# Optimization experiments

Hardware: AMD Instinct MI355X
Metric: run time of the kernel (lower is better)

Reference implementation:

```python
import jax, jax.numpy as jnp
import numpy as np

T, B, D = 4096, 64, 64
SCALE = D ** (-0.5)


def setup_inputs() -> dict:
    key = jax.random.key(0)
    ks = jax.random.split(key, 8)
    init = 1.0 / np.sqrt(D)  # mimic nn.Linear default scale roughly
    return {
        "eeg": jax.random.normal(ks[0], (T, B, D), dtype=jnp.float32),
        "fnirs": jax.random.normal(ks[1], (T, B, D), dtype=jnp.float32),
        "Wq": jax.random.normal(ks[2], (D, D), dtype=jnp.float32) * init,
        "bq": jax.random.normal(ks[3], (D,), dtype=jnp.float32) * init,
        "Wk": jax.random.normal(ks[4], (D, D), dtype=jnp.float32) * init,
        "bk": jax.random.normal(ks[5], (D,), dtype=jnp.float32) * init,
        "Wv": jax.random.normal(ks[6], (D, D), dtype=jnp.float32) * init,
        "bv": jax.random.normal(ks[7], (D,), dtype=jnp.float32) * init,
    }


def reference(eeg, fnirs, Wq, bq, Wk, bk, Wv, bv):
    # Linear layers: x @ W.T + b (torch nn.Linear convention, W is [out, in])
    q = jnp.einsum("tbd,od->tbo", eeg, Wq) + bq      # [T, B, D]
    k = jnp.einsum("tbd,od->tbo", fnirs, Wk) + bk    # [T, B, D]
    v = jnp.einsum("tbd,od->tbo", fnirs, Wv) + bv    # [T, B, D]
    # Elementwise QK gating score, summed over feature dim -> [T, B, 1]
    score = jnp.sum(q * k, axis=-1, keepdims=True) * SCALE
    # Softmax over the sequence axis (dim=0)
    attn = jax.nn.softmax(score, axis=0)
    # Residual combine
    return eeg + attn * v
```

## Files before the change

kernel.cpp:

```cpp
#include <hip/hip_runtime.h>
#include <hip/hip_bf16.h>
#include <math.h>

#define T_DIM 4096
#define B_DIM 64
#define D_DIM 64
#define NROWS (T_DIM * B_DIM)
#define NTILES (NROWS / 16)

#define WS_M     0
#define WS_W     4096
#define WS_U     4160
#define WS_C     4224
#define WS_SCORE 8192

typedef __attribute__((ext_vector_type(4))) float f32x4;
typedef __attribute__((ext_vector_type(8))) short bf16x8;

static __device__ inline short f2bf(float x) {
  union { float f; unsigned u; } v; v.f = x;
  return (short)((v.u + 0x7FFFu + ((v.u >> 16) & 1u)) >> 16);
}

static __device__ inline bf16x8 load_cvt8(const float* __restrict__ p) {
  const float4 a = *reinterpret_cast<const float4*>(p);
  const float4 b = *reinterpret_cast<const float4*>(p + 4);
  bf16x8 r;
  r[0] = f2bf(a.x); r[1] = f2bf(a.y); r[2] = f2bf(a.z); r[3] = f2bf(a.w);
  r[4] = f2bf(b.x); r[5] = f2bf(b.y); r[6] = f2bf(b.z); r[7] = f2bf(b.w);
  return r;
}

__global__ __launch_bounds__(64) void k1_precompute(
    const float* __restrict__ Wq, const float* __restrict__ bq,
    const float* __restrict__ Wk, const float* __restrict__ bk,
    float* __restrict__ ws) {
  const int tid = threadIdx.x;
  const int blk = blockIdx.x;
  if (blk < 64) {
    const int d = blk;
    float acc = 0.f;
    for (int o = 0; o < 64; ++o)
      acc = fmaf(Wq[o * 64 + d], Wk[o * 64 + tid], acc);
    ws[WS_M + d * 64 + tid] = acc;
  } else {
    float uacc = 0.f, wacc = 0.f, cacc = 0.f;
    for (int o = 0; o < 64; ++o) {
      uacc = fmaf(bq[o], Wk[o * 64 + tid], uacc);
      wacc = fmaf(Wq[o * 64 + tid], bk[o], wacc);
      cacc = fmaf(bq[o], bk[o], cacc);
    }
    ws[WS_U + tid] = uacc;
    ws[WS_W + tid] = wacc;
    if (tid == 0) ws[WS_C] = cacc;
  }
}

__global__ __launch_bounds__(256, 4) void k2_score_mfma(
    const float* __restrict__ eeg, const float* __restrict__ fnirs,
    const float* __restrict__ Mm, const float* __restrict__ wvec,
    const float* __restrict__ uvec, const float* __restrict__ cvec,
    float* __restrict__ score) {
  const int lane = threadIdx.x & 63;
  const int wv   = threadIdx.x >> 6;
  const int wid  = blockIdx.x * 4 + wv;
  const int nwav = gridDim.x * 4;
  const int col  = lane & 15;
  const int grp  = lane >> 4;
  const int kb   = grp * 8;

  bf16x8 bf[5][2];
#pragma unroll
  for (int ct = 0; ct < 4; ++ct) {
    const int c = ct * 16 + col;
#pragma unroll
    for (int kf = 0; kf < 2; ++kf)
      bf[ct][kf] = load_cvt8(Mm + c * 64 + kf * 32 + kb);
  }
#pragma unroll
  for (int kf = 0; kf < 2; ++kf) {
    bf16x8 z = (bf16x8)(short)0;
    if (col == 0) z = load_cvt8(uvec + kf * 32 + kb);
    bf[4][kf] = z;
  }
  const float wreg[4] = { wvec[col], wvec[16 + col], wvec[32 + col], wvec[48 + col] };
  const float cb = cvec[0];
  const f32x4 zero = {0.f, 0.f, 0.f, 0.f};

  for (int tile = wid; tile < NTILES; tile += nwav) {
    const int rbase = tile * 16;
    const float* fa = fnirs + (size_t)(rbase + col) * 64 + kb;
    const bf16x8 a0 = load_cvt8(fa);
    const bf16x8 a1 = load_cvt8(fa + 32);
    f32x4 acc[5];
#pragma unroll
    for (int ct = 0; ct < 5; ++ct) {
      acc[ct] = __builtin_amdgcn_mfma_f32_16x16x32_bf16(a0, bf[ct][0], zero, 0, 0, 0);
      acc[ct] = __builtin_amdgcn_mfma_f32_16x16x32_bf16(a1, bf[ct][1], acc[ct], 0, 0, 0);
    }
    float partial[4];
#pragma unroll
    for (int i = 0; i < 4; ++i) {
      const int row = rbase + grp * 4 + i;
      float s = 0.f;
#pragma unroll
      for (int ct = 0; ct < 4; ++ct) {
        const float e = eeg[(size_t)row * 64 + ct * 16 + col];
        s = fmaf(e, acc[ct][i] + wreg[ct], s);
      }
      if (col == 0) s += acc[4][i] + cb;
      partial[i] = s;
    }
#pragma unroll
    for (int m = 8; m >= 1; m >>= 1) {
#pragma unroll
      for (int i = 0; i < 4; ++i)
        partial[i] += __shfl_xor(partial[i], m, 64);
    }
    if (col == 0) {
      float4 o = { partial[0] * 0.125f, partial[1] * 0.125f,
                   partial[2] * 0.125f, partial[3] * 0.125f };
      *reinterpret_cast<float4*>(score + rbase + grp * 4) = o;
    }
  }
}

__global__ __launch_bounds__(256) void k3_softmax(float* __restrict__ sc) {
  __shared__ float red[8];
  __shared__ float sinv;
  const int b = blockIdx.x;
  const int tid = threadIdx.x;

  float vals[16];
  float m = -1e30f;
#pragma unroll
  for (int k = 0; k < 16; ++k) {
    vals[k] = sc[(size_t)(k * 256 + tid) * 64 + b];
    m = fmaxf(m, vals[k]);
  }
#pragma unroll
  for (int off = 32; off > 0; off >>= 1)
    m = fmaxf(m, __shfl_xor(m, off, 64));
  if ((tid & 63) == 0) red[tid >> 6] = m;
  __syncthreads();
  m = fmaxf(fmaxf(red[0], red[1]), fmaxf(red[2], red[3]));

  float s = 0.f;
#pragma unroll
  for (int k = 0; k < 16; ++k) s += __expf(vals[k] - m);
#pragma unroll
  for (int off = 32; off > 0; off >>= 1)
    s += __shfl_xor(s, off, 64);
  if ((tid & 63) == 0) red[4 + (tid >> 6)] = s;
  __syncthreads();
  if (tid == 0) sinv = 1.0f / (red[4] + red[5] + red[6] + red[7]);
  __syncthreads();
  const float inv = sinv;
#pragma unroll
  for (int k = 0; k < 16; ++k)
    sc[(size_t)(k * 256 + tid) * 64 + b] = __expf(vals[k] - m) * inv;
}

__global__ __launch_bounds__(256, 4) void k4_output_mfma(
    const float* __restrict__ eeg, const float* __restrict__ fnirs,
    const float* __restrict__ Wv, const float* __restrict__ bv,
    const float* __restrict__ attn, float* __restrict__ out) {
  const int lane = threadIdx.x & 63;
  const int wv   = threadIdx.x >> 6;
  const int wid  = blockIdx.x * 4 + wv;
  const int nwav = gridDim.x * 4;
  const int col  = lane & 15;
  const int grp  = lane >> 4;
  const int kb   = grp * 8;

  bf16x8 bf[4][2];
#pragma unroll
  for (int ct = 0; ct < 4; ++ct) {
    const int c = ct * 16 + col;
#pragma unroll
    for (int kf = 0; kf < 2; ++kf)
      bf[ct][kf] = load_cvt8(Wv + c * 64 + kf * 32 + kb);
  }
  const float bvreg[4] = { bv[col], bv[16 + col], bv[32 + col], bv[48 + col] };
  const f32x4 zero = {0.f, 0.f, 0.f, 0.f};

  for (int tile = wid; tile < NTILES; tile += nwav) {
    const int rbase = tile * 16;
    const float* fa = fnirs + (size_t)(rbase + col) * 64 + kb;
    const bf16x8 a0 = load_cvt8(fa);
    const bf16x8 a1 = load_cvt8(fa + 32);
    f32x4 acc[4];
#pragma unroll
    for (int ct = 0; ct < 4; ++ct) {
      acc[ct] = __builtin_amdgcn_mfma_f32_16x16x32_bf16(a0, bf[ct][0], zero, 0, 0, 0);
      acc[ct] = __builtin_amdgcn_mfma_f32_16x16x32_bf16(a1, bf[ct][1], acc[ct], 0, 0, 0);
    }
    const float4 a4 = *reinterpret_cast<const float4*>(attn + rbase + grp * 4);
    const float av[4] = { a4.x, a4.y, a4.z, a4.w };
#pragma unroll
    for (int i = 0; i < 4; ++i) {
      const size_t row = rbase + grp * 4 + i;
#pragma unroll
      for (int ct = 0; ct < 4; ++ct) {
        const float e = eeg[row * 64 + ct * 16 + col];
        out[row * 64 + ct * 16 + col] = fmaf(av[i], acc[ct][i] + bvreg[ct], e);
      }
    }
  }
}

extern "C" void kernel_launch(void* const* d_in, const int* in_sizes, int n_in,
                              void* d_out, int out_size, void* d_ws, size_t ws_size,
                              hipStream_t stream) {
  const float* eeg   = (const float*)d_in[0];
  const float* fnirs = (const float*)d_in[1];
  const float* Wq    = (const float*)d_in[2];
  const float* bq    = (const float*)d_in[3];
  const float* Wk    = (const float*)d_in[4];
  const float* bk    = (const float*)d_in[5];
  const float* Wv    = (const float*)d_in[6];
  const float* bv    = (const float*)d_in[7];
  float* out = (float*)d_out;
  float* ws  = (float*)d_ws;

  k1_precompute<<<65, 64, 0, stream>>>(Wq, bq, Wk, bk, ws);
  k2_score_mfma<<<1024, 256, 0, stream>>>(eeg, fnirs,
                                          ws + WS_M, ws + WS_W, ws + WS_U,
                                          ws + WS_C, ws + WS_SCORE);
  k3_softmax<<<64, 256, 0, stream>>>(ws + WS_SCORE);
  k4_output_mfma<<<1024, 256, 0, stream>>>(eeg, fnirs, Wv, bv,
                                           ws + WS_SCORE, out);
}
```

Measured before the change: 81.72 us.

## Precompute bf16 weights and use one-tile-per-wave grids with front-loaded loads

The precompute kernel now writes the folded QK matrix, the u vector and Wv as bf16 into the workspace. The score and output kernels load these bf16 fragments directly instead of converting fp32 weights in every wave. Both MFMA kernels drop the persistent grid-stride loop and launch one 16-row tile per wave (4096 blocks), issuing all fnirs, eeg and attn loads up front so more memory requests are in flight. The cost is more blocks and a repeated weight load per wave, plus eeg values held in registers.

Result: faster. 79.63 us (-2.6%).

```diff
diff --git a/kernel.cpp b/kernel.cpp
--- a/kernel.cpp
+++ b/kernel.cpp
@@ -8,9 +8,10 @@
 #define NROWS (T_DIM * B_DIM)
 #define NTILES (NROWS / 16)
 
-#define WS_M     0
-#define WS_W     4096
-#define WS_U     4160
+#define WS_MBF   0
+#define WS_VBF   2048
+#define WS_UBF   4096
+#define WS_W     4160
 #define WS_C     4224
 #define WS_SCORE 8192
 
@@ -18,13 +19,11 @@
 typedef __attribute__((ext_vector_type(8))) short bf16x8;
 
 static __device__ inline short f2bf(float x) {
-  union { float f; unsigned u; } v; v.f = x;
-  return (short)((v.u + 0x7FFFu + ((v.u >> 16) & 1u)) >> 16);
-}
-
-static __device__ inline bf16x8 load_cvt8(const float* __restrict__ p) {
-  const float4 a = *reinterpret_cast<const float4*>(p);
-  const float4 b = *reinterpret_cast<const float4*>(p + 4);
+  __hip_bfloat16 h = __float2bfloat16(x);
+  return *reinterpret_cast<short*>(&h);
+}
+
+static __device__ inline bf16x8 cvt8(const float4 a, const float4 b) {
   bf16x8 r;
   r[0] = f2bf(a.x); r[1] = f2bf(a.y); r[2] = f2bf(a.z); r[3] = f2bf(a.w);
   r[4] = f2bf(b.x); r[5] = f2bf(b.y); r[6] = f2bf(b.z); r[7] = f2bf(b.w);
@@ -34,15 +33,19 @@
 __global__ __launch_bounds__(64) void k1_precompute(
     const float* __restrict__ Wq, const float* __restrict__ bq,
     const float* __restrict__ Wk, const float* __restrict__ bk,
-    float* __restrict__ ws) {
+    const float* __restrict__ Wv, float* __restrict__ ws) {
   const int tid = threadIdx.x;
   const int blk = blockIdx.x;
+  unsigned short* __restrict__ mbf = (unsigned short*)(ws + WS_MBF);
+  unsigned short* __restrict__ vbf = (unsigned short*)(ws + WS_VBF);
+  unsigned short* __restrict__ ubf = (unsigned short*)(ws + WS_UBF);
   if (blk < 64) {
     const int d = blk;
     float acc = 0.f;
     for (int o = 0; o < 64; ++o)
       acc = fmaf(Wq[o * 64 + d], Wk[o * 64 + tid], acc);
-    ws[WS_M + d * 64 + tid] = acc;
+    mbf[d * 64 + tid] = (unsigned short)f2bf(acc);
+    vbf[d * 64 + tid] = (unsigned short)f2bf(Wv[d * 64 + tid]);
   } else {
     float uacc = 0.f, wacc = 0.f, cacc = 0.f;
     for (int o = 0; o < 64; ++o) {
@@ -50,7 +53,7 @@
       wacc = fmaf(Wq[o * 64 + tid], bk[o], wacc);
       cacc = fmaf(bq[o], bk[o], cacc);
     }
-    ws[WS_U + tid] = uacc;
+    ubf[tid] = (unsigned short)f2bf(uacc);
     ws[WS_W + tid] = wacc;
     if (tid == 0) ws[WS_C] = cacc;
   }
@@ -58,70 +61,75 @@
 
 __global__ __launch_bounds__(256, 4) void k2_score_mfma(
     const float* __restrict__ eeg, const float* __restrict__ fnirs,
-    const float* __restrict__ Mm, const float* __restrict__ wvec,
-    const float* __restrict__ uvec, const float* __restrict__ cvec,
+    const unsigned short* __restrict__ mbf, const float* __restrict__ wvec,
+    const unsigned short* __restrict__ ubf, const float* __restrict__ cvec,
     float* __restrict__ score) {
   const int lane = threadIdx.x & 63;
   const int wv   = threadIdx.x >> 6;
-  const int wid  = blockIdx.x * 4 + wv;
-  const int nwav = gridDim.x * 4;
+  const int tile = blockIdx.x * 4 + wv;
   const int col  = lane & 15;
   const int grp  = lane >> 4;
   const int kb   = grp * 8;
-
-  bf16x8 bf[5][2];
-#pragma unroll
-  for (int ct = 0; ct < 4; ++ct) {
-    const int c = ct * 16 + col;
+  const int rbase = tile * 16;
+
+  const float* fa = fnirs + (size_t)(rbase + col) * 64 + kb;
+  const float4 f0a = *reinterpret_cast<const float4*>(fa);
+  const float4 f0b = *reinterpret_cast<const float4*>(fa + 4);
+  const float4 f1a = *reinterpret_cast<const float4*>(fa + 32);
+  const float4 f1b = *reinterpret_cast<const float4*>(fa + 36);
+  float ee[4][4];
+#pragma unroll
+  for (int i = 0; i < 4; ++i)
+#pragma unroll
+    for (int ct = 0; ct < 4; ++ct)
+      ee[i][ct] = eeg[(size_t)(rbase + grp * 4 + i) * 64 + ct * 16 + col];
+
+  bf16x8 bm[5][2];
+#pragma unroll
+  for (int ct = 0; ct < 4; ++ct)
 #pragma unroll
     for (int kf = 0; kf < 2; ++kf)
-      bf[ct][kf] = load_cvt8(Mm + c * 64 + kf * 32 + kb);
-  }
+      bm[ct][kf] = *reinterpret_cast<const bf16x8*>(
+          mbf + (ct * 16 + col) * 64 + kf * 32 + kb);
 #pragma unroll
   for (int kf = 0; kf < 2; ++kf) {
     bf16x8 z = (bf16x8)(short)0;
-    if (col == 0) z = load_cvt8(uvec + kf * 32 + kb);
-    bf[4][kf] = z;
+    if (col == 0)
+      z = *reinterpret_cast<const bf16x8*>(ubf + kf * 32 + kb);
+    bm[4][kf] = z;
   }
   const float wreg[4] = { wvec[col], wvec[16 + col], wvec[32 + col], wvec[48 + col] };
   const float cb = cvec[0];
+
+  const bf16x8 a0 = cvt8(f0a, f0b);
+  const bf16x8 a1 = cvt8(f1a, f1b);
   const f32x4 zero = {0.f, 0.f, 0.f, 0.f};
-
-  for (int tile = wid; tile < NTILES; tile += nwav) {
-    const int rbase = tile * 16;
-    const float* fa = fnirs + (size_t)(rbase + col) * 64 + kb;
-    const bf16x8 a0 = load_cvt8(fa);
-    const bf16x8 a1 = load_cvt8(fa + 32);
-    f32x4 acc[5];
-#pragma unroll
-    for (int ct = 0; ct < 5; ++ct) {
-      acc[ct] = __builtin_amdgcn_mfma_f32_16x16x32_bf16(a0, bf[ct][0], zero, 0, 0, 0);
-      acc[ct] = __builtin_amdgcn_mfma_f32_16x16x32_bf16(a1, bf[ct][1], acc[ct], 0, 0, 0);
-    }
-    float partial[4];
-#pragma unroll
-    for (int i = 0; i < 4; ++i) {
-      const int row = rbase + grp * 4 + i;
-      float s = 0.f;
-#pragma unroll
-      for (int ct = 0; ct < 4; ++ct) {
-        const float e = eeg[(size_t)row * 64 + ct * 16 + col];
-        s = fmaf(e, acc[ct][i] + wreg[ct], s);
-      }
-      if (col == 0) s += acc[4][i] + cb;
-      partial[i] = s;
-    }
-#pragma unroll
-    for (int m = 8; m >= 1; m >>= 1) {
-#pragma unroll
-      for (int i = 0; i < 4; ++i)
-        partial[i] += __shfl_xor(partial[i], m, 64);
-    }
-    if (col == 0) {
-      float4 o = { partial[0] * 0.125f, partial[1] * 0.125f,
-                   partial[2] * 0.125f, partial[3] * 0.125f };
-      *reinterpret_cast<float4*>(score + rbase + grp * 4) = o;
-    }
+  f32x4 acc[5];
+#pragma unroll
+  for (int ct = 0; ct < 5; ++ct) {
+    acc[ct] = __builtin_amdgcn_mfma_f32_16x16x32_bf16(a0, bm[ct][0], zero, 0, 0, 0);
+    acc[ct] = __builtin_amdgcn_mfma_f32_16x16x32_bf16(a1, bm[ct][1], acc[ct], 0, 0, 0);
+  }
+
+  float partial[4];
+#pragma unroll
+  for (int i = 0; i < 4; ++i) {
+    float s = 0.f;
+#pragma unroll
+    for (int ct = 0; ct < 4; ++ct)
+      s = fmaf(ee[i][ct], acc[ct][i] + wreg[ct], s);
+    if (col == 0) s += acc[4][i] + cb;
+    partial[i] = s;
+  }
+#pragma unroll
+  for (int m = 8; m >= 1; m >>= 1)
+#pragma unroll
+    for (int i = 0; i < 4; ++i)
+      partial[i] += __shfl_xor(partial[i], m, 64);
+  if (col == 0) {
+    float4 o = { partial[0] * 0.125f, partial[1] * 0.125f,
+                 partial[2] * 0.125f, partial[3] * 0.125f };
+    *reinterpret_cast<float4*>(score + rbase + grp * 4) = o;
   }
 }
 
@@ -163,49 +171,55 @@
 
 __global__ __launch_bounds__(256, 4) void k4_output_mfma(
     const float* __restrict__ eeg, const float* __restrict__ fnirs,
-    const float* __restrict__ Wv, const float* __restrict__ bv,
+    const unsigned short* __restrict__ vbf, const float* __restrict__ bv,
     const float* __restrict__ attn, float* __restrict__ out) {
   const int lane = threadIdx.x & 63;
   const int wv   = threadIdx.x >> 6;
-  const int wid  = blockIdx.x * 4 + wv;
-  const int nwav = gridDim.x * 4;
+  const int tile = blockIdx.x * 4 + wv;
   const int col  = lane & 15;
   const int grp  = lane >> 4;
   const int kb   = grp * 8;
-
-  bf16x8 bf[4][2];
+  const int rbase = tile * 16;
+
+  const float* fa = fnirs + (size_t)(rbase + col) * 64 + kb;
+  const float4 f0a = *reinterpret_cast<const float4*>(fa);
+  const float4 f0b = *reinterpret_cast<const float4*>(fa + 4);
+  const float4 f1a = *reinterpret_cast<const float4*>(fa + 32);
+  const float4 f1b = *reinterpret_cast<const float4*>(fa + 36);
+  float ee[4][4];
+#pragma unroll
+  for (int i = 0; i < 4; ++i)
+#pragma unroll
+    for (int ct = 0; ct < 4; ++ct)
+      ee[i][ct] = eeg[(size_t)(rbase + grp * 4 + i) * 64 + ct * 16 + col];
+  const float4 a4 = *reinterpret_cast<const float4*>(attn + rbase + grp * 4);
+
+  bf16x8 bm[4][2];
+#pragma unroll
+  for (int ct = 0; ct < 4; ++ct)
+#pragma unroll
+    for (int kf = 0; kf < 2; ++kf)
+      bm[ct][kf] = *reinterpret_cast<const bf16x8*>(
+          vbf + (ct * 16 + col) * 64 + kf * 32 + kb);
+  const float bvreg[4] = { bv[col], bv[16 + col], bv[32 + col], bv[48 + col] };
+
+  const bf16x8 a0 = cvt8(f0a, f0b);
+  const bf16x8 a1 = cvt8(f1a, f1b);
+  const f32x4 zero = {0.f, 0.f, 0.f, 0.f};
+  f32x4 acc[4];
 #pragma unroll
   for (int ct = 0; ct < 4; ++ct) {
-    const int c = ct * 16 + col;
-#pragma unroll
-    for (int kf = 0; kf < 2; ++kf)
-      bf[ct][kf] = load_cvt8(Wv + c * 64 + kf * 32 + kb);
-  }
-  const float bvreg[4] = { bv[col], bv[16 + col], bv[32 + col], bv[48 + col] };
-  const f32x4 zero = {0.f, 0.f, 0.f, 0.f};
-
-  for (int tile = wid; tile < NTILES; tile += nwav) {
-    const int rbase = tile * 16;
-    const float* fa = fnirs + (size_t)(rbase + col) * 64 + kb;
-    const bf16x8 a0 = load_cvt8(fa);
-    const bf16x8 a1 = load_cvt8(fa + 32);
-    f32x4 acc[4];
-#pragma unroll
-    for (int ct = 0; ct < 4; ++ct) {
-      acc[ct] = __builtin_amdgcn_mfma_f32_16x16x32_bf16(a0, bf[ct][0], zero, 0, 0, 0);
-      acc[ct] = __builtin_amdgcn_mfma_f32_16x16x32_bf16(a1, bf[ct][1], acc[ct], 0, 0, 0);
-    }
-    const float4 a4 = *reinterpret_cast<const float4*>(attn + rbase + grp * 4);
-    const float av[4] = { a4.x, a4.y, a4.z, a4.w };
-#pragma unroll
-    for (int i = 0; i < 4; ++i) {
-      const size_t row = rbase + grp * 4 + i;
-#pragma unroll
-      for (int ct = 0; ct < 4; ++ct) {
-        const float e = eeg[row * 64 + ct * 16 + col];
-        out[row * 64 + ct * 16 + col] = fmaf(av[i], acc[ct][i] + bvreg[ct], e);
-      }
-    }
+    acc[ct] = __builtin_amdgcn_mfma_f32_16x16x32_bf16(a0, bm[ct][0], zero, 0, 0, 0);
+    acc[ct] = __builtin_amdgcn_mfma_f32_16x16x32_bf16(a1, bm[ct][1], acc[ct], 0, 0, 0);
+  }
+
+  const float av[4] = { a4.x, a4.y, a4.z, a4.w };
+#pragma unroll
+  for (int i = 0; i < 4; ++i) {
+    const size_t row = rbase + grp * 4 + i;
+#pragma unroll
+    for (int ct = 0; ct < 4; ++ct)
+      out[row * 64 + ct * 16 + col] = fmaf(av[i], acc[ct][i] + bvreg[ct], ee[i][ct]);
   }
 }
 
@@ -223,11 +237,13 @@
   float* out = (float*)d_out;
   float* ws  = (float*)d_ws;
 
-  k1_precompute<<<65, 64, 0, stream>>>(Wq, bq, Wk, bk, ws);
-  k2_score_mfma<<<1024, 256, 0, stream>>>(eeg, fnirs,
-                                          ws + WS_M, ws + WS_W, ws + WS_U,
-                                          ws + WS_C, ws + WS_SCORE);
+  k1_precompute<<<65, 64, 0, stream>>>(Wq, bq, Wk, bk, Wv, ws);
+  k2_score_mfma<<<NTILES / 4, 256, 0, stream>>>(
+      eeg, fnirs,
+      (const unsigned short*)(ws + WS_MBF), ws + WS_W,
+      (const unsigned short*)(ws + WS_UBF), ws + WS_C, ws + WS_SCORE);
   k3_softmax<<<64, 256, 0, stream>>>(ws + WS_SCORE);
-  k4_output_mfma<<<1024, 256, 0, stream>>>(eeg, fnirs, Wv, bv,
-                                           ws + WS_SCORE, out);
-}
+  k4_output_mfma<<<NTILES / 4, 256, 0, stream>>>(
+      eeg, fnirs, (const unsigned short*)(ws + WS_VBF), bv,
+      ws + WS_SCORE, out);
+}
```
